# Optimization experiments

Hardware: AMD Instinct MI355X
Metric: run time of the kernel (lower is better)

The kernel has to match this reference:

```python
import jax, jax.numpy as jnp
import numpy as np

N_NODES = 32768
N_EDGES = 65536
IN_DIM = 3      # node feature / edge attr dim (input_size)
HID = 64        # NNConv hidden/out channels
FC1 = 128


def setup_inputs() -> dict:
    key = jax.random.key(0)
    ks = jax.random.split(key, 16)
    inp = {}
    inp["x"] = jax.random.normal(ks[0], (N_NODES, IN_DIM), dtype=jnp.float32)
    inp["edge_index"] = jax.random.randint(ks[1], (2, N_EDGES), 0, N_NODES, dtype=jnp.int64)
    inp["edge_attr"] = jax.random.normal(ks[2], (N_EDGES, IN_DIM), dtype=jnp.float32)
    s = lambda fi, fo: 1.0 / np.sqrt(fi)
    # edge MLP 1: IN_DIM -> 64 -> IN_DIM*HID
    inp["W1a"] = jax.random.normal(ks[3], (IN_DIM, 64), dtype=jnp.float32) * s(IN_DIM, 64)
    inp["b1a"] = jnp.zeros((64,), dtype=jnp.float32)
    inp["W1b"] = jax.random.normal(ks[4], (64, IN_DIM * HID), dtype=jnp.float32) * s(64, IN_DIM * HID)
    inp["b1b"] = jnp.zeros((IN_DIM * HID,), dtype=jnp.float32)
    inp["root1"] = jax.random.normal(ks[5], (IN_DIM, HID), dtype=jnp.float32) * s(IN_DIM, HID)
    inp["bias1"] = jnp.zeros((HID,), dtype=jnp.float32)
    # edge MLP 2: IN_DIM -> 64 -> HID*HID
    inp["W2a"] = jax.random.normal(ks[6], (IN_DIM, 64), dtype=jnp.float32) * s(IN_DIM, 64)
    inp["b2a"] = jnp.zeros((64,), dtype=jnp.float32)
    inp["W2b"] = jax.random.normal(ks[7], (64, HID * HID), dtype=jnp.float32) * s(64, HID * HID)
    inp["b2b"] = jnp.zeros((HID * HID,), dtype=jnp.float32)
    inp["root2"] = jax.random.normal(ks[8], (HID, HID), dtype=jnp.float32) * s(HID, HID)
    inp["bias2"] = jnp.zeros((HID,), dtype=jnp.float32)
    # fc1
    inp["Wf"] = jax.random.normal(ks[9], (HID, FC1), dtype=jnp.float32) * s(HID, FC1)
    inp["bf"] = jnp.zeros((FC1,), dtype=jnp.float32)
    return inp


def _nnconv(x, src, dst, edge_attr, Wa, ba, Wb, bb, root, bias, in_c, out_c):
    # per-edge weight matrix from edge MLP: [E, in_c, out_c]
    h = jax.nn.relu(edge_attr @ Wa + ba)
    W_e = (h @ Wb + bb).reshape(-1, in_c, out_c)
    # gather source features, transform per edge: [E, out_c]
    msg = jnp.einsum('ei,eio->eo', x[src], W_e)
    # scatter-mean into target nodes
    summed = jax.ops.segment_sum(msg, dst, num_segments=N_NODES)
    cnt = jax.ops.segment_sum(jnp.ones((msg.shape[0],), msg.dtype), dst, num_segments=N_NODES)
    agg = summed / jnp.maximum(cnt, 1.0)[:, None]
    return agg + x @ root + bias


def reference(x, edge_index, edge_attr, W1a, b1a, W1b, b1b, root1, bias1,
              W2a, b2a, W2b, b2b, root2, bias2, Wf, bf):
    src, dst = edge_index[0], edge_index[1]
    h = jax.nn.elu(_nnconv(x, src, dst, edge_attr, W1a, b1a, W1b, b1b, root1, bias1, IN_DIM, HID))
    h = jax.nn.elu(_nnconv(h, src, dst, edge_attr, W2a, b2a, W2b, b2b, root2, bias2, HID, HID))
    h = jax.nn.elu(h @ Wf + bf)
    # dropout is identity in eval mode
    return h
```

## Files before the change

### kernel.cpp

```cpp
#include <hip/hip_runtime.h>
#include <math.h>

#define NN 32768
#define NE 65536

typedef __attribute__((ext_vector_type(8))) short bf16x8;
typedef __attribute__((ext_vector_type(4))) float f32x4;

__device__ __forceinline__ float elu_f(float v) {
    return v > 0.f ? v : (expf(v) - 1.f);
}
__device__ __forceinline__ unsigned short bf16_rn(float f) {
    unsigned u = __float_as_uint(f);
    return (unsigned short)((u + 0x7FFFu + ((u >> 16) & 1u)) >> 16);
}
__device__ __forceinline__ float bf16_to_f(unsigned short h) {
    return __uint_as_float(((unsigned)h) << 16);
}
__device__ __forceinline__ void gld16(const void* g, void* l) {
    __builtin_amdgcn_global_load_lds(
        (const __attribute__((address_space(1))) unsigned int*)g,
        (__attribute__((address_space(3))) unsigned int*)l, 16, 0, 0);
}

#define FMA8(Cj, aj, b0, b1) \
    Cj[0] += (aj)*(b0).x; Cj[1] += (aj)*(b0).y; Cj[2] += (aj)*(b0).z; Cj[3] += (aj)*(b0).w; \
    Cj[4] += (aj)*(b1).x; Cj[5] += (aj)*(b1).y; Cj[6] += (aj)*(b1).z; Cj[7] += (aj)*(b1).w;

__global__ void k_prep2(const float* __restrict__ W2b, const float* __restrict__ b2b,
                        const float* __restrict__ W1b, const int* __restrict__ ei,
                        short* __restrict__ BT2, short* __restrict__ BT1,
                        int* __restrict__ cnt) {
    int g = blockIdx.x * 256 + threadIdx.x;
    if (g < 262144) {
        float f = W2b[g];
        int o = g & 63, i = (g >> 6) & 63, k = g >> 12;
        unsigned short hi = bf16_rn(f);
        unsigned short lo = bf16_rn(f - bf16_to_f(hi));
        BT2[(size_t)k * 9216 + o * 72 + i]        = (short)hi;
        BT2[(size_t)k * 9216 + 4608 + o * 72 + i] = (short)lo;
    } else if (g < 266240) {
        int g2 = g - 262144;
        float f = b2b[g2];
        int o = g2 & 63, i = g2 >> 6;
        unsigned short hi = bf16_rn(f);
        unsigned short lo = bf16_rn(f - bf16_to_f(hi));
        BT2[(size_t)64 * 9216 + o * 72 + i]        = (short)hi;
        BT2[(size_t)64 * 9216 + 4608 + o * 72 + i] = (short)lo;
    } else if (g < 278528) {
        int g2 = g - 266240;
        float f = W1b[g2];
        int col = g2 % 192, k = g2 / 192;
        int c = col >> 6, o = col & 63;
        unsigned short hi = bf16_rn(f);
        unsigned short lo = bf16_rn(f - bf16_to_f(hi));
        BT1[c * 9216 + o * 72 + k]        = (short)hi;
        BT1[c * 9216 + 4608 + o * 72 + k] = (short)lo;
    } else {
        int e = g - 278528;
        atomicAdd(&cnt[ei[NE + e]], 1);
    }
}

__global__ __launch_bounds__(1024) void k_scan(const int* __restrict__ cnt,
                                               int* __restrict__ start,
                                               int* __restrict__ cursor) {
    __shared__ int wtot[16];
    const int t = threadIdx.x;
    const int lane = t & 63, wave = t >> 6;
    int local[32];
    const int base = t * 32;
    int s = 0;
    #pragma unroll
    for (int j = 0; j < 32; ++j) { local[j] = s; s += cnt[base + j]; }
    const int tot = s;
    int sc = tot;
    #pragma unroll
    for (int off = 1; off < 64; off <<= 1) {
        int v = __shfl_up(sc, off, 64);
        if (lane >= off) sc += v;
    }
    if (lane == 63) wtot[wave] = sc;
    __syncthreads();
    if (t == 0) {
        int run = 0;
        #pragma unroll
        for (int w = 0; w < 16; ++w) { int v = wtot[w]; wtot[w] = run; run += v; }
    }
    __syncthreads();
    const int tbase = wtot[wave] + (sc - tot);
    #pragma unroll
    for (int j = 0; j < 32; ++j) {
        int v = tbase + local[j];
        start[base + j] = v;
        cursor[base + j] = v;
    }
}

__global__ void k_fill(const int* __restrict__ ei, int* __restrict__ cursor,
                       int* __restrict__ perm) {
    int e = blockIdx.x * 256 + threadIdx.x;
    if (e < NE) {
        int d = ei[NE + e];
        int pos = atomicAdd(&cursor[d], 1);
        perm[pos] = e;
    }
}

__global__ __launch_bounds__(256, 2) void k1_conv1(
    const float* __restrict__ x, const int* __restrict__ ei,
    const float* __restrict__ eatt,
    const float* __restrict__ W1a, const float* __restrict__ b1a,
    const short* __restrict__ BT1, const float* __restrict__ b1b,
    float* __restrict__ msg1)
{
    __shared__ __align__(16) short sBT1[3 * 9216];
    __shared__ float sxs[128 * 4];
    __shared__ float sea[128 * 4];
    __shared__ float sW1a[192];
    __shared__ float sb1a[64];
    __shared__ float sb1b[192];

    const int tid = threadIdx.x;
    const int e0  = blockIdx.x * 128;
    const int wid = tid >> 6;
    const int lane = tid & 63;
    const int l15 = lane & 15, lhi = lane >> 4;

    {
        const char* src = (const char*)BT1;
        char* dst = (char*)&sBT1[0];
        for (int j = wid; j < 54; j += 4)
            gld16(src + j * 1024 + lane * 16, dst + j * 1024);
    }
    if (tid < 192) { sW1a[tid] = W1a[tid]; sb1b[tid] = b1b[tid]; }
    if (tid < 64)  sb1a[tid] = b1a[tid];
    if (tid < 128) {
        int e = e0 + tid;
        int s = ei[e];
        sxs[tid*4+0] = x[s*3+0];
        sxs[tid*4+1] = x[s*3+1];
        sxs[tid*4+2] = x[s*3+2];
        sea[tid*4+0] = eatt[e*3+0];
        sea[tid*4+1] = eatt[e*3+1];
        sea[tid*4+2] = eatt[e*3+2];
    }
    __syncthreads();

    bf16x8 ah[2][2], al[2][2];
    #pragma unroll
    for (int rt = 0; rt < 2; ++rt) {
        const int arow = wid*32 + rt*16 + l15;
        const float a0 = sea[arow*4+0], a1 = sea[arow*4+1], a2 = sea[arow*4+2];
        #pragma unroll
        for (int kc = 0; kc < 2; ++kc) {
            const int kb = kc*32 + lhi*8;
            bf16x8 H, L;
            #pragma unroll
            for (int j = 0; j < 8; ++j) {
                int k = kb + j;
                float f = fmaxf(sb1a[k] + a0*sW1a[k] + a1*sW1a[64+k] + a2*sW1a[128+k], 0.f);
                unsigned short hh = bf16_rn(f);
                unsigned short ll = bf16_rn(f - bf16_to_f(hh));
                H[j] = (short)hh; L[j] = (short)ll;
            }
            ah[rt][kc] = H; al[rt][kc] = L;
        }
    }
    float xr[2][4][3];
    #pragma unroll
    for (int rt = 0; rt < 2; ++rt)
        #pragma unroll
        for (int r = 0; r < 4; ++r) {
            int crow = wid*32 + rt*16 + lhi*4 + r;
            xr[rt][r][0] = sxs[crow*4+0];
            xr[rt][r][1] = sxs[crow*4+1];
            xr[rt][r][2] = sxs[crow*4+2];
        }

    f32x4 acc[2][4];
    #pragma unroll
    for (int rt = 0; rt < 2; ++rt)
        #pragma unroll
        for (int ot = 0; ot < 4; ++ot) { acc[rt][ot][0]=0.f; acc[rt][ot][1]=0.f; acc[rt][ot][2]=0.f; acc[rt][ot][3]=0.f; }

    #pragma unroll
    for (int c = 0; c < 3; ++c) {
        const short* Bh = &sBT1[c * 9216];
        const short* Bl = Bh + 4608;
        #pragma unroll
        for (int ot = 0; ot < 4; ++ot) {
            const int ob = (ot*16 + l15)*72 + lhi*8;
            bf16x8 bh0 = *(const bf16x8*)&Bh[ob];
            bf16x8 bh1 = *(const bf16x8*)&Bh[ob + 32];
            bf16x8 bl0 = *(const bf16x8*)&Bl[ob];
            bf16x8 bl1 = *(const bf16x8*)&Bl[ob + 32];
            #pragma unroll
            for (int rt = 0; rt < 2; ++rt) {
                f32x4 t = {0.f, 0.f, 0.f, 0.f};
                t = __builtin_amdgcn_mfma_f32_16x16x32_bf16(ah[rt][0], bh0, t, 0, 0, 0);
                t = __builtin_amdgcn_mfma_f32_16x16x32_bf16(al[rt][0], bh0, t, 0, 0, 0);
                t = __builtin_amdgcn_mfma_f32_16x16x32_bf16(ah[rt][0], bl0, t, 0, 0, 0);
                t = __builtin_amdgcn_mfma_f32_16x16x32_bf16(ah[rt][1], bh1, t, 0, 0, 0);
                t = __builtin_amdgcn_mfma_f32_16x16x32_bf16(al[rt][1], bh1, t, 0, 0, 0);
                t = __builtin_amdgcn_mfma_f32_16x16x32_bf16(ah[rt][1], bl1, t, 0, 0, 0);
                #pragma unroll
                for (int r = 0; r < 4; ++r)
                    acc[rt][ot][r] += xr[rt][r][c] * t[r];
            }
        }
    }
    #pragma unroll
    for (int rt = 0; rt < 2; ++rt) {
        #pragma unroll
        for (int ot = 0; ot < 4; ++ot) {
            const int o = ot*16 + l15;
            const float b0 = sb1b[o], b1 = sb1b[64+o], b2 = sb1b[128+o];
            #pragma unroll
            for (int r = 0; r < 4; ++r) {
                float v = acc[rt][ot][r] + xr[rt][r][0]*b0 + xr[rt][r][1]*b1 + xr[rt][r][2]*b2;
                int row = e0 + wid*32 + rt*16 + lhi*4 + r;
                msg1[(size_t)row * 64 + o] = v;
            }
        }
    }
}

__global__ __launch_bounds__(256) void k2_node1(
    const float* __restrict__ msg1, const int* __restrict__ start,
    const int* __restrict__ cnt, const int* __restrict__ perm,
    const float* __restrict__ x, const float* __restrict__ root1,
    const float* __restrict__ bias1, float* __restrict__ h1)
{
    __shared__ float sR[192], sb[64];
    const int tid = threadIdx.x;
    if (tid < 192) sR[tid] = root1[tid];
    if (tid < 64)  sb[tid] = bias1[tid];
    __syncthreads();
    const int n = blockIdx.x * 64 + (tid >> 2);
    const int c = (tid & 3) * 16;
    const int st = start[n], num = cnt[n];
    float acc[16];
    #pragma unroll
    for (int l = 0; l < 16; ++l) acc[l] = 0.f;
    for (int d = 0; d < num; ++d) {
        const int row = perm[st + d];
        const float* rp = &msg1[(size_t)row * 64 + c];
        #pragma unroll
        for (int q = 0; q < 4; ++q) {
            float4 v = *(const float4*)(rp + q * 4);
            acc[q*4+0] += v.x; acc[q*4+1] += v.y; acc[q*4+2] += v.z; acc[q*4+3] += v.w;
        }
    }
    const float inv = 1.f / fmaxf((float)num, 1.f);
    const float x0 = x[n*3+0], x1 = x[n*3+1], x2 = x[n*3+2];
    float* hp = &h1[(size_t)n * 64 + c];
    #pragma unroll
    for (int q = 0; q < 4; ++q) {
        float4 ov;
        float* o4 = (float*)&ov;
        #pragma unroll
        for (int l = 0; l < 4; ++l) {
            int o = c + q*4 + l;
            float v = acc[q*4+l] * inv + sb[o] + x0*sR[o] + x1*sR[64+o] + x2*sR[128+o];
            o4[l] = elu_f(v);
        }
        *(float4*)(hp + q*4) = ov;
    }
}

__global__ __launch_bounds__(256, 2) void k3_mfma(
    const float* __restrict__ h1, const int* __restrict__ ei,
    const float* __restrict__ eatt,
    const float* __restrict__ W2a, const float* __restrict__ b2a,
    const short* __restrict__ BT2,
    float* __restrict__ msg2)
{
    __shared__ __align__(16) float sV[128 * 68];
    __shared__ __align__(16) short sB[2][9216];
    __shared__ float sea[128 * 4];
    __shared__ float sW2a[192];
    __shared__ float sb2a[64];

    const int tid = threadIdx.x;
    const int e0  = blockIdx.x * 128;
    const int wid = tid >> 6;
    const int lane = tid & 63;
    const int l15 = lane & 15, lhi = lane >> 4;

    {
        const char* src = (const char*)BT2;
        char* dst = (char*)&sB[0][0];
        for (int j = wid; j < 18; j += 4)
            gld16(src + j * 1024 + lane * 16, dst + j * 1024);
    }
    if (tid < 192) sW2a[tid] = W2a[tid];
    if (tid < 64)  sb2a[tid] = b2a[tid];
    if (tid < 128) {
        int e = e0 + tid;
        sea[tid*4+0] = eatt[e*3+0];
        sea[tid*4+1] = eatt[e*3+1];
        sea[tid*4+2] = eatt[e*3+2];
    }
    {
        const int edge = tid >> 1, half = tid & 1;
        const int s = ei[e0 + edge];
        const float* row = h1 + (size_t)s * 64 + half * 32;
        float* dst = &sV[edge * 68 + half * 32];
        #pragma unroll
        for (int q = 0; q < 8; ++q)
            *(float4*)(dst + q*4) = *(const float4*)(row + q*4);
    }
    __syncthreads();

    bf16x8 vh[2][2], vl[2][2];
    #pragma unroll
    for (int rt = 0; rt < 2; ++rt)
        #pragma unroll
        for (int kc = 0; kc < 2; ++kc) {
            const float* p = &sV[(wid*32 + rt*16 + l15)*68 + kc*32 + lhi*8];
            bf16x8 H, L;
            #pragma unroll
            for (int j = 0; j < 8; ++j) {
                float f = p[j];
                unsigned short hh = bf16_rn(f);
                unsigned short ll = bf16_rn(f - bf16_to_f(hh));
                H[j] = (short)hh; L[j] = (short)ll;
            }
            vh[rt][kc] = H; vl[rt][kc] = L;
        }
    float er[2][4][3];
    #pragma unroll
    for (int rt = 0; rt < 2; ++rt)
        #pragma unroll
        for (int r = 0; r < 4; ++r) {
            int row = wid*32 + rt*16 + lhi*4 + r;
            er[rt][r][0] = sea[row*4+0];
            er[rt][r][1] = sea[row*4+1];
            er[rt][r][2] = sea[row*4+2];
        }

    f32x4 acc[2][4];
    #pragma unroll
    for (int rt = 0; rt < 2; ++rt)
        #pragma unroll
        for (int ot = 0; ot < 4; ++ot) { acc[rt][ot][0]=0.f; acc[rt][ot][1]=0.f; acc[rt][ot][2]=0.f; acc[rt][ot][3]=0.f; }

    int cur = 0;
    for (int k = 0; k <= 64; ++k) {
        if (k < 64) {
            const char* src = (const char*)(BT2 + (size_t)(k + 1) * 9216);
            char* dst = (char*)&sB[cur ^ 1][0];
            for (int j = wid; j < 18; j += 4)
                gld16(src + j * 1024 + lane * 16, dst + j * 1024);
        }
        float us[2][4];
        if (k < 64) {
            const float wa = sW2a[k], wb = sW2a[64+k], wc = sW2a[128+k], bb = sb2a[k];
            #pragma unroll
            for (int rt = 0; rt < 2; ++rt)
                #pragma unroll
                for (int r = 0; r < 4; ++r)
                    us[rt][r] = fmaxf(bb + er[rt][r][0]*wa + er[rt][r][1]*wb + er[rt][r][2]*wc, 0.f);
        } else {
            #pragma unroll
            for (int rt = 0; rt < 2; ++rt)
                #pragma unroll
                for (int r = 0; r < 4; ++r) us[rt][r] = 1.f;
        }
        const short* Bh = &sB[cur][0];
        const short* Bl = &sB[cur][4608];
        #pragma unroll
        for (int ot = 0; ot < 4; ++ot) {
            const int ob = (ot*16 + l15)*72 + lhi*8;
            bf16x8 bh0 = *(const bf16x8*)&Bh[ob];
            bf16x8 bh1 = *(const bf16x8*)&Bh[ob + 32];
            bf16x8 bl0 = *(const bf16x8*)&Bl[ob];
            bf16x8 bl1 = *(const bf16x8*)&Bl[ob + 32];
            #pragma unroll
            for (int rt = 0; rt < 2; ++rt) {
                f32x4 t = {0.f, 0.f, 0.f, 0.f};
                t = __builtin_amdgcn_mfma_f32_16x16x32_bf16(vh[rt][0], bh0, t, 0, 0, 0);
                t = __builtin_amdgcn_mfma_f32_16x16x32_bf16(vl[rt][0], bh0, t, 0, 0, 0);
                t = __builtin_amdgcn_mfma_f32_16x16x32_bf16(vh[rt][0], bl0, t, 0, 0, 0);
                t = __builtin_amdgcn_mfma_f32_16x16x32_bf16(vh[rt][1], bh1, t, 0, 0, 0);
                t = __builtin_amdgcn_mfma_f32_16x16x32_bf16(vl[rt][1], bh1, t, 0, 0, 0);
                t = __builtin_amdgcn_mfma_f32_16x16x32_bf16(vh[rt][1], bl1, t, 0, 0, 0);
                #pragma unroll
                for (int r = 0; r < 4; ++r)
                    acc[rt][ot][r] += us[rt][r] * t[r];
            }
        }
        __syncthreads();
        if (k < 64) cur ^= 1;
    }

    #pragma unroll
    for (int rt = 0; rt < 2; ++rt)
        #pragma unroll
        for (int ot = 0; ot < 4; ++ot) {
            const int o = ot*16 + l15;
            #pragma unroll
            for (int r = 0; r < 4; ++r) {
                int row = e0 + wid*32 + rt*16 + lhi*4 + r;
                msg2[(size_t)row * 64 + o] = acc[rt][ot][r];
            }
        }
}

__global__ __launch_bounds__(256, 2) void k4_final(
    const float* __restrict__ msg2, const int* __restrict__ start,
    const int* __restrict__ cnt, const int* __restrict__ perm,
    const float* __restrict__ h1,
    const float* __restrict__ root2, const float* __restrict__ bias2,
    const float* __restrict__ Wf, const float* __restrict__ bf,
    float* __restrict__ out)
{
    __shared__ float sh1[32 * 65];
    __shared__ float sh2[32 * 65];
    __shared__ float sR[64 * 64];
    __shared__ float sW[64 * 128];
    __shared__ float sb2[64];
    __shared__ float sbf[128];
    __shared__ float sinv[32];
    __shared__ int   sstart[32];
    __shared__ int   scnt[32];
    const int tid = threadIdx.x;
    const int n0 = blockIdx.x * 32;

    for (int u = tid; u < 64*64/4; u += 256) ((float4*)sR)[u] = ((const float4*)root2)[u];
    for (int u = tid; u < 64*128/4; u += 256) ((float4*)sW)[u] = ((const float4*)Wf)[u];
    if (tid < 64)  sb2[tid] = bias2[tid];
    if (tid < 128) sbf[tid] = bf[tid];
    if (tid < 32) {
        int n = n0 + tid;
        int cc = cnt[n];
        sstart[tid] = start[n];
        scnt[tid] = cc;
        sinv[tid] = 1.f / fmaxf((float)cc, 1.f);
    }
    for (int u = tid; u < 32 * 16; u += 256) {
        int n = u >> 4, i4 = (u & 15) * 4;
        float4 v = *(const float4*)&h1[(size_t)(n0 + n) * 64 + i4];
        sh1[n*65+i4] = v.x; sh1[n*65+i4+1] = v.y; sh1[n*65+i4+2] = v.z; sh1[n*65+i4+3] = v.w;
    }
    __syncthreads();

    {
        const int tn = tid >> 4;
        const int o0 = (tid & 15) * 4;
        float acc[2][4];
        #pragma unroll
        for (int j = 0; j < 2; ++j) {
            int ln = tn * 2 + j;
            int st = sstart[ln], num = scnt[ln];
            float4 a = {0.f, 0.f, 0.f, 0.f};
            for (int d = 0; d < num; ++d) {
                int row = perm[st + d];
                float4 s = *(const float4*)&msg2[(size_t)row * 64 + o0];
                a.x += s.x; a.y += s.y; a.z += s.z; a.w += s.w;
            }
            float inv = sinv[ln];
            acc[j][0] = a.x*inv + sb2[o0+0];
            acc[j][1] = a.y*inv + sb2[o0+1];
            acc[j][2] = a.z*inv + sb2[o0+2];
            acc[j][3] = a.w*inv + sb2[o0+3];
        }
        #pragma unroll 8
        for (int k = 0; k < 64; ++k) {
            float4 r = *(const float4*)&sR[k*64 + o0];
            float h0 = sh1[(tn*2)*65 + k];
            float h1v = sh1[(tn*2+1)*65 + k];
            acc[0][0] += h0*r.x; acc[0][1] += h0*r.y; acc[0][2] += h0*r.z; acc[0][3] += h0*r.w;
            acc[1][0] += h1v*r.x; acc[1][1] += h1v*r.y; acc[1][2] += h1v*r.z; acc[1][3] += h1v*r.w;
        }
        #pragma unroll
        for (int j = 0; j < 2; ++j) {
            int n = tn * 2 + j;
            #pragma unroll
            for (int l = 0; l < 4; ++l) sh2[n*65 + o0 + l] = elu_f(acc[j][l]);
        }
    }
    __syncthreads();

    {
        const int tn = tid >> 4;
        const int c0 = (tid & 15) * 8;
        float acc[2][8];
        #pragma unroll
        for (int j = 0; j < 2; ++j)
            #pragma unroll
            for (int l = 0; l < 8; ++l) acc[j][l] = sbf[c0 + l];
        #pragma unroll 8
        for (int k = 0; k < 64; ++k) {
            float4 w0 = *(const float4*)&sW[k*128 + c0];
            float4 w1 = *(const float4*)&sW[k*128 + c0 + 4];
            float h0 = sh2[(tn*2)*65 + k];
            float h1v = sh2[(tn*2+1)*65 + k];
            FMA8(acc[0], h0, w0, w1);
            FMA8(acc[1], h1v, w0, w1);
        }
        #pragma unroll
        for (int j = 0; j < 2; ++j) {
            size_t n = n0 + tn * 2 + j;
            float4 oA, oB;
            oA.x = elu_f(acc[j][0]); oA.y = elu_f(acc[j][1]); oA.z = elu_f(acc[j][2]); oA.w = elu_f(acc[j][3]);
            oB.x = elu_f(acc[j][4]); oB.y = elu_f(acc[j][5]); oB.z = elu_f(acc[j][6]); oB.w = elu_f(acc[j][7]);
            *(float4*)&out[n*128 + c0]     = oA;
            *(float4*)&out[n*128 + c0 + 4] = oB;
        }
    }
}

extern "C" void kernel_launch(void* const* d_in, const int* in_sizes, int n_in,
                              void* d_out, int out_size, void* d_ws, size_t ws_size,
                              hipStream_t stream)
{
    const float* x     = (const float*)d_in[0];
    const int*   ei    = (const int*)d_in[1];
    const float* ea    = (const float*)d_in[2];
    const float* W1a   = (const float*)d_in[3];
    const float* b1a   = (const float*)d_in[4];
    const float* W1b   = (const float*)d_in[5];
    const float* b1b   = (const float*)d_in[6];
    const float* root1 = (const float*)d_in[7];
    const float* bias1 = (const float*)d_in[8];
    const float* W2a   = (const float*)d_in[9];
    const float* b2a   = (const float*)d_in[10];
    const float* W2b   = (const float*)d_in[11];
    const float* b2b   = (const float*)d_in[12];
    const float* root2 = (const float*)d_in[13];
    const float* bias2 = (const float*)d_in[14];
    const float* Wf    = (const float*)d_in[15];
    const float* bf    = (const float*)d_in[16];
    float* out = (float*)d_out;

    float* ws    = (float*)d_ws;
    float* msg1  = ws;
    float* msg2  = ws + 4194304;
    float* h1    = ws + 8388608;
    short* BT2   = (short*)(ws + 10485760);
    short* BT1   = (short*)(ws + 10785280);
    int*   cnt_i = (int*)(ws + 10799104);
    int*   startp= (int*)(ws + 10831872);
    int*   cursor= (int*)(ws + 10864640);
    int*   perm  = (int*)(ws + 10897408);

    hipMemsetAsync(cnt_i, 0, (size_t)NN * sizeof(int), stream);

    k_prep2 <<<1344,      256, 0, stream>>>(W2b, b2b, W1b, ei, BT2, BT1, cnt_i);
    k_scan  <<<1,        1024, 0, stream>>>(cnt_i, startp, cursor);
    k_fill  <<<NE/256,    256, 0, stream>>>(ei, cursor, perm);
    k1_conv1<<<NE/128,    256, 0, stream>>>(x, ei, ea, W1a, b1a, BT1, b1b, msg1);
    k2_node1<<<NN/64,     256, 0, stream>>>(msg1, startp, cnt_i, perm, x, root1, bias1, h1);
    k3_mfma <<<NE/128,    256, 0, stream>>>(h1, ei, ea, W2a, b2a, BT2, msg2);
    k4_final<<<NN/32,     256, 0, stream>>>(msg2, startp, cnt_i, perm, h1, root2, bias2, Wf, bf, out);
}
```

Before: 268.7 us.

## Load per-k weight fragments directly into registers, drop LDS staging and barriers

The edge-conditioned weight slices for the second NNConv are now read straight from global memory (L2-resident, shared by all blocks) into register fragments. A two-deep register double buffer replaces the LDS double buffer, which removes the per-k __syncthreads and the 36 KB shared buffer. The prep kernel's packed layout drops its padding to match. This raises register pressure (32 extra bf16x8 fragments) and relies on cache bandwidth for repeated per-wave global loads, but it may allow higher occupancy and no block-wide sync.

```diff
diff --git a/kernel.cpp b/kernel.cpp
--- a/kernel.cpp
+++ b/kernel.cpp
@@ -37,16 +37,16 @@
         int o = g & 63, i = (g >> 6) & 63, k = g >> 12;
         unsigned short hi = bf16_rn(f);
         unsigned short lo = bf16_rn(f - bf16_to_f(hi));
-        BT2[(size_t)k * 9216 + o * 72 + i]        = (short)hi;
-        BT2[(size_t)k * 9216 + 4608 + o * 72 + i] = (short)lo;
+        BT2[(size_t)k * 8192 + o * 64 + i]        = (short)hi;
+        BT2[(size_t)k * 8192 + 4096 + o * 64 + i] = (short)lo;
     } else if (g < 266240) {
         int g2 = g - 262144;
         float f = b2b[g2];
         int o = g2 & 63, i = g2 >> 6;
         unsigned short hi = bf16_rn(f);
         unsigned short lo = bf16_rn(f - bf16_to_f(hi));
-        BT2[(size_t)64 * 9216 + o * 72 + i]        = (short)hi;
-        BT2[(size_t)64 * 9216 + 4608 + o * 72 + i] = (short)lo;
+        BT2[(size_t)64 * 8192 + o * 64 + i]        = (short)hi;
+        BT2[(size_t)64 * 8192 + 4096 + o * 64 + i] = (short)lo;
     } else if (g < 278528) {
         int g2 = g - 266240;
         float f = W1b[g2];
@@ -277,7 +277,6 @@
     float* __restrict__ msg2)
 {
     __shared__ __align__(16) float sV[128 * 68];
-    __shared__ __align__(16) short sB[2][9216];
     __shared__ float sea[128 * 4];
     __shared__ float sW2a[192];
     __shared__ float sb2a[64];
@@ -288,12 +287,6 @@
     const int lane = tid & 63;
     const int l15 = lane & 15, lhi = lane >> 4;
 
-    {
-        const char* src = (const char*)BT2;
-        char* dst = (char*)&sB[0][0];
-        for (int j = wid; j < 18; j += 4)
-            gld16(src + j * 1024 + lane * 16, dst + j * 1024);
-    }
     if (tid < 192) sW2a[tid] = W2a[tid];
     if (tid < 64)  sb2a[tid] = b2a[tid];
     if (tid < 128) {
@@ -346,54 +339,70 @@
         #pragma unroll
         for (int ot = 0; ot < 4; ++ot) { acc[rt][ot][0]=0.f; acc[rt][ot][1]=0.f; acc[rt][ot][2]=0.f; acc[rt][ot][3]=0.f; }
 
-    int cur = 0;
-    for (int k = 0; k <= 64; ++k) {
-        if (k < 64) {
-            const char* src = (const char*)(BT2 + (size_t)(k + 1) * 9216);
-            char* dst = (char*)&sB[cur ^ 1][0];
-            for (int j = wid; j < 18; j += 4)
-                gld16(src + j * 1024 + lane * 16, dst + j * 1024);
-        }
-        float us[2][4];
-        if (k < 64) {
-            const float wa = sW2a[k], wb = sW2a[64+k], wc = sW2a[128+k], bb = sb2a[k];
-            #pragma unroll
-            for (int rt = 0; rt < 2; ++rt)
-                #pragma unroll
-                for (int r = 0; r < 4; ++r)
-                    us[rt][r] = fmaxf(bb + er[rt][r][0]*wa + er[rt][r][1]*wb + er[rt][r][2]*wc, 0.f);
-        } else {
-            #pragma unroll
-            for (int rt = 0; rt < 2; ++rt)
-                #pragma unroll
-                for (int r = 0; r < 4; ++r) us[rt][r] = 1.f;
-        }
-        const short* Bh = &sB[cur][0];
-        const short* Bl = &sB[cur][4608];
-        #pragma unroll
-        for (int ot = 0; ot < 4; ++ot) {
-            const int ob = (ot*16 + l15)*72 + lhi*8;
-            bf16x8 bh0 = *(const bf16x8*)&Bh[ob];
-            bf16x8 bh1 = *(const bf16x8*)&Bh[ob + 32];
-            bf16x8 bl0 = *(const bf16x8*)&Bl[ob];
-            bf16x8 bl1 = *(const bf16x8*)&Bl[ob + 32];
-            #pragma unroll
-            for (int rt = 0; rt < 2; ++rt) {
-                f32x4 t = {0.f, 0.f, 0.f, 0.f};
-                t = __builtin_amdgcn_mfma_f32_16x16x32_bf16(vh[rt][0], bh0, t, 0, 0, 0);
-                t = __builtin_amdgcn_mfma_f32_16x16x32_bf16(vl[rt][0], bh0, t, 0, 0, 0);
-                t = __builtin_amdgcn_mfma_f32_16x16x32_bf16(vh[rt][0], bl0, t, 0, 0, 0);
-                t = __builtin_amdgcn_mfma_f32_16x16x32_bf16(vh[rt][1], bh1, t, 0, 0, 0);
-                t = __builtin_amdgcn_mfma_f32_16x16x32_bf16(vl[rt][1], bh1, t, 0, 0, 0);
-                t = __builtin_amdgcn_mfma_f32_16x16x32_bf16(vh[rt][1], bl1, t, 0, 0, 0);
-                #pragma unroll
-                for (int r = 0; r < 4; ++r)
-                    acc[rt][ot][r] += us[rt][r] * t[r];
-            }
-        }
-        __syncthreads();
-        if (k < 64) cur ^= 1;
-    }
+    int boff[4];
+    #pragma unroll
+    for (int ot = 0; ot < 4; ++ot) boff[ot] = (ot*16 + l15)*64 + lhi*8;
+
+    #define LOADB(dst, kk)                                                        \
+        {                                                                         \
+            const short* p_ = BT2 + (size_t)(kk) * 8192;                          \
+            _Pragma("unroll")                                                     \
+            for (int ot = 0; ot < 4; ++ot) {                                      \
+                dst[ot][0] = *(const bf16x8*)(p_ + boff[ot]);                     \
+                dst[ot][1] = *(const bf16x8*)(p_ + boff[ot] + 32);                \
+                dst[ot][2] = *(const bf16x8*)(p_ + boff[ot] + 4096);              \
+                dst[ot][3] = *(const bf16x8*)(p_ + boff[ot] + 4096 + 32);         \
+            }                                                                     \
+        }
+
+    #define STEP(frag, kk)                                                        \
+        {                                                                         \
+            float us_[2][4];                                                      \
+            if ((kk) < 64) {                                                      \
+                const float wa = sW2a[(kk)], wb = sW2a[64+(kk)],                  \
+                            wc = sW2a[128+(kk)], bb = sb2a[(kk)];                 \
+                _Pragma("unroll")                                                 \
+                for (int rt = 0; rt < 2; ++rt)                                    \
+                    _Pragma("unroll")                                             \
+                    for (int r = 0; r < 4; ++r)                                   \
+                        us_[rt][r] = fmaxf(bb + er[rt][r][0]*wa +                 \
+                                           er[rt][r][1]*wb + er[rt][r][2]*wc, 0.f);\
+            } else {                                                              \
+                _Pragma("unroll")                                                 \
+                for (int rt = 0; rt < 2; ++rt)                                    \
+                    _Pragma("unroll")                                             \
+                    for (int r = 0; r < 4; ++r) us_[rt][r] = 1.f;                 \
+            }                                                                     \
+            _Pragma("unroll")                                                     \
+            for (int ot = 0; ot < 4; ++ot) {                                      \
+                _Pragma("unroll")                                                 \
+                for (int rt = 0; rt < 2; ++rt) {                                  \
+                    f32x4 t = {0.f, 0.f, 0.f, 0.f};                               \
+                    t = __builtin_amdgcn_mfma_f32_16x16x32_bf16(vh[rt][0], frag[ot][0], t, 0, 0, 0); \
+                    t = __builtin_amdgcn_mfma_f32_16x16x32_bf16(vl[rt][0], frag[ot][0], t, 0, 0, 0); \
+                    t = __builtin_amdgcn_mfma_f32_16x16x32_bf16(vh[rt][0], frag[ot][2], t, 0, 0, 0); \
+                    t = __builtin_amdgcn_mfma_f32_16x16x32_bf16(vh[rt][1], frag[ot][1], t, 0, 0, 0); \
+                    t = __builtin_amdgcn_mfma_f32_16x16x32_bf16(vl[rt][1], frag[ot][1], t, 0, 0, 0); \
+                    t = __builtin_amdgcn_mfma_f32_16x16x32_bf16(vh[rt][1], frag[ot][3], t, 0, 0, 0); \
+                    _Pragma("unroll")                                             \
+                    for (int r = 0; r < 4; ++r)                                   \
+                        acc[rt][ot][r] += us_[rt][r] * t[r];                      \
+                }                                                                 \
+            }                                                                     \
+        }
+
+    bf16x8 ba[4][4], bb2[4][4];
+    LOADB(ba, 0);
+    for (int k = 0; k < 64; k += 2) {
+        LOADB(bb2, k + 1);
+        STEP(ba, k);
+        LOADB(ba, k + 2);
+        STEP(bb2, k + 1);
+    }
+    STEP(ba, 64);
+
+    #undef LOADB
+    #undef STEP
 
     #pragma unroll
     for (int rt = 0; rt < 2; ++rt)
```

Result: slower. 414.1 us (+54.1%).
